# Optimization experiments

Measured on AMD Instinct MI355X. Metric: run time of the kernel, lower is better.

## Reference

```python
import jax, jax.numpy as jnp
import numpy as np

POOL_SIZE = 7
NUM_ROIS = 1000
H, W, C = 128, 128, 1024


def setup_inputs() -> dict:
    key = jax.random.key(0)
    k_img, k_xy, k_wh = jax.random.split(key, 3)
    img = jax.random.normal(k_img, (1, H, W, C), dtype=jnp.float32)
    # rois[0, i] = (x, y, w, h) in feature-map pixel units; ensure x+w<=W, y+h<=H
    xy = jax.random.randint(k_xy, (1, NUM_ROIS, 2), 0, 64, dtype=jnp.int32)
    wh = jax.random.randint(k_wh, (1, NUM_ROIS, 2), 8, 65, dtype=jnp.int32)
    rois = jnp.concatenate([xy, wh], axis=-1)  # [1, num_rois, 4]
    return {"img": img, "rois": rois}


def _axis_coords(start, size, out_size):
    """Half-pixel-center bilinear source coords for a crop [start, start+size).

    Matches tf.image.resize(method='bilinear', antialias=False): src = (i+0.5)*scale - 0.5,
    clamped to the crop, then split into floor index / +1 index / lerp weight.
    """
    size_f = size.astype(jnp.float32)
    f = (jnp.arange(out_size, dtype=jnp.float32) + 0.5) * (size_f / out_size) - 0.5
    f = jnp.clip(f, 0.0, jnp.maximum(size_f - 1.0, 0.0))
    i0 = jnp.floor(f).astype(jnp.int32)
    i1 = jnp.minimum(i0 + 1, size - 1)
    wgt = f - i0.astype(jnp.float32)
    return start + i0, start + i1, wgt


def _pool_one_roi(img2d, roi):
    # img2d: [H, W, C]; roi: [4] int32 (x, y, w, h)
    x, y, w, h = roi[0], roi[1], roi[2], roi[3]
    y0, y1, wy = _axis_coords(y, h, POOL_SIZE)  # each [P]
    x0, x1, wx = _axis_coords(x, w, POOL_SIZE)
    v00 = img2d[y0[:, None], x0[None, :], :]  # [P, P, C]
    v01 = img2d[y0[:, None], x1[None, :], :]
    v10 = img2d[y1[:, None], x0[None, :], :]
    v11 = img2d[y1[:, None], x1[None, :], :]
    wy = wy[:, None, None]
    wx = wx[None, :, None]
    top = v00 * (1.0 - wx) + v01 * wx
    bot = v10 * (1.0 - wx) + v11 * wx
    return top * (1.0 - wy) + bot * wy


def reference(img, rois):
    # Vectorized RoiPoolingConv.call: batched crop + bilinear resize over all ROIs.
    pooled = jax.vmap(_pool_one_roi, in_axes=(None, 0))(img[0], rois[0])  # [R, P, P, C]
    return pooled[None]  # [1, num_rois, P, P, C]
```

## Files before the change

kernel.cpp:

```cpp
#include <hip/hip_runtime.h>

#define POOL 7
#define NROIS 1000
#define NCELLS (NROIS * POOL * POOL)
#define IMG_W 128
#define NCH 1024
#define NXCD 8
#define CG_CH 128
#define CELLS_PER_BLK 8
#define NBLK_PER_XCD (NCELLS / CELLS_PER_BLK)

typedef float f4 __attribute__((ext_vector_type(4)));

__global__ __launch_bounds__(256) void roi_pool_kernel(
    const float* __restrict__ img,
    const int* __restrict__ rois,
    float* __restrict__ out)
{
    const unsigned bid  = blockIdx.x;
    const unsigned xcd  = bid & 7u;
    const unsigned cblk = bid >> 3;
    const unsigned t    = threadIdx.x;
    const unsigned cell = cblk * CELLS_PER_BLK + (t >> 5);
    const unsigned lane = t & 31u;

    const unsigned roi = cell / 49u;
    const unsigned c49 = cell - roi * 49u;
    const unsigned py  = c49 / 7u;
    const unsigned px  = c49 - py * 7u;

    const int4 r = ((const int4*)rois)[roi];
    const int x = r.x, y = r.y, w = r.z, h = r.w;

    const float hf = (float)h;
    float fy = ((float)py + 0.5f) * (hf / (float)POOL) - 0.5f;
    fy = fminf(fmaxf(fy, 0.0f), fmaxf(hf - 1.0f, 0.0f));
    const int   iy0 = (int)floorf(fy);
    const int   iy1 = min(iy0 + 1, h - 1);
    const float wy  = fy - (float)iy0;
    const int   y0  = y + iy0;
    const int   y1  = y + iy1;

    const float wf = (float)w;
    float fx = ((float)px + 0.5f) * (wf / (float)POOL) - 0.5f;
    fx = fminf(fmaxf(fx, 0.0f), fmaxf(wf - 1.0f, 0.0f));
    const int   ix0 = (int)floorf(fx);
    const int   ix1 = min(ix0 + 1, w - 1);
    const float wx  = fx - (float)ix0;
    const int   x0  = x + ix0;
    const int   x1  = x + ix1;

    const unsigned choff = xcd * CG_CH + lane * 4u;

    const f4* p00 = (const f4*)(img + ((size_t)y0 * IMG_W + x0) * NCH + choff);
    const f4* p01 = (const f4*)(img + ((size_t)y0 * IMG_W + x1) * NCH + choff);
    const f4* p10 = (const f4*)(img + ((size_t)y1 * IMG_W + x0) * NCH + choff);
    const f4* p11 = (const f4*)(img + ((size_t)y1 * IMG_W + x1) * NCH + choff);
    f4* po = (f4*)(out + (size_t)cell * NCH + choff);

    const f4 a = *p00;
    const f4 b = *p01;
    const f4 c = *p10;
    const f4 d = *p11;

    const float owx = 1.0f - wx;
    const float owy = 1.0f - wy;

    const f4 top = a * owx + b * wx;
    const f4 bot = c * owx + d * wx;
    const f4 res = top * owy + bot * wy;

    __builtin_nontemporal_store(res, po);
}

extern "C" void kernel_launch(void* const* d_in, const int* in_sizes, int n_in,
                              void* d_out, int out_size, void* d_ws, size_t ws_size,
                              hipStream_t stream)
{
    const float* img  = (const float*)d_in[0];
    const int*   rois = (const int*)d_in[1];
    float*       out  = (float*)d_out;

    const int nblocks = NBLK_PER_XCD * NXCD;
    roi_pool_kernel<<<nblocks, 256, 0, stream>>>(img, rois, out);
}
```

Measured before the change: 277.0 us.

## Sort ROIs by y-coordinate before pooling to improve cache locality

Adds a single-block counting-sort kernel that buckets ROIs by their y origin, writing sorted ROI records and a permutation into workspace. The pooling kernel then processes ROIs in sorted order, so neighbouring blocks gather from nearby image rows, and it scatters each result back to the original ROI slot. The aim is better L2/MALL reuse of the 64MB image across concurrently running blocks. The cost is an extra tiny kernel launch, a serial dependency between the two kernels, and output writes that are no longer sequential across blocks.

```diff
diff --git a/kernel.cpp b/kernel.cpp
--- a/kernel.cpp
+++ b/kernel.cpp
@@ -12,24 +12,51 @@
 
 typedef float f4 __attribute__((ext_vector_type(4)));
 
+__global__ __launch_bounds__(256) void roi_sort_kernel(
+    const int* __restrict__ rois, int4* __restrict__ sorted,
+    int* __restrict__ perm)
+{
+    __shared__ int hist[64];
+    __shared__ int base[64];
+    const int t = threadIdx.x;
+    if (t < 64) hist[t] = 0;
+    __syncthreads();
+    for (int i = t; i < NROIS; i += 256)
+        atomicAdd(&hist[rois[4 * i + 1] & 63], 1);
+    __syncthreads();
+    if (t == 0) {
+        int acc = 0;
+        for (int b = 0; b < 64; ++b) { base[b] = acc; acc += hist[b]; }
+    }
+    __syncthreads();
+    for (int i = t; i < NROIS; i += 256) {
+        const int4 r = ((const int4*)rois)[i];
+        const int pos = atomicAdd(&base[r.y & 63], 1);
+        sorted[pos] = r;
+        perm[pos] = i;
+    }
+}
+
 __global__ __launch_bounds__(256) void roi_pool_kernel(
     const float* __restrict__ img,
-    const int* __restrict__ rois,
+    const int4* __restrict__ sorted,
+    const int* __restrict__ perm,
     float* __restrict__ out)
 {
     const unsigned bid  = blockIdx.x;
     const unsigned xcd  = bid & 7u;
     const unsigned cblk = bid >> 3;
     const unsigned t    = threadIdx.x;
-    const unsigned cell = cblk * CELLS_PER_BLK + (t >> 5);
+    const unsigned sc   = cblk * CELLS_PER_BLK + (t >> 5);
     const unsigned lane = t & 31u;
 
-    const unsigned roi = cell / 49u;
-    const unsigned c49 = cell - roi * 49u;
-    const unsigned py  = c49 / 7u;
-    const unsigned px  = c49 - py * 7u;
+    const unsigned rank = sc / 49u;
+    const unsigned c49  = sc - rank * 49u;
+    const unsigned py   = c49 / 7u;
+    const unsigned px   = c49 - py * 7u;
 
-    const int4 r = ((const int4*)rois)[roi];
+    const int4 r   = sorted[rank];
+    const int orig = perm[rank];
     const int x = r.x, y = r.y, w = r.z, h = r.w;
 
     const float hf = (float)h;
@@ -56,6 +83,8 @@
     const f4* p01 = (const f4*)(img + ((size_t)y0 * IMG_W + x1) * NCH + choff);
     const f4* p10 = (const f4*)(img + ((size_t)y1 * IMG_W + x0) * NCH + choff);
     const f4* p11 = (const f4*)(img + ((size_t)y1 * IMG_W + x1) * NCH + choff);
+
+    const unsigned cell = (unsigned)orig * 49u + c49;
     f4* po = (f4*)(out + (size_t)cell * NCH + choff);
 
     const f4 a = *p00;
@@ -81,6 +110,11 @@
     const int*   rois = (const int*)d_in[1];
     float*       out  = (float*)d_out;
 
+    int4* sorted = (int4*)d_ws;
+    int*  perm   = (int*)((char*)d_ws + NROIS * 16);
+
+    roi_sort_kernel<<<1, 256, 0, stream>>>(rois, sorted, perm);
+
     const int nblocks = NBLK_PER_XCD * NXCD;
-    roi_pool_kernel<<<nblocks, 256, 0, stream>>>(img, rois, out);
+    roi_pool_kernel<<<nblocks, 256, 0, stream>>>(img, sorted, perm, out);
 }
```

New measurement: 286.8 us. 3.5% more time.
